# Optimization experiments

Hardware: AMD Instinct MI355X
Metric: run time of the kernel (lower is better)

## Reference

```python
import jax, jax.numpy as jnp
import numpy as np

S = 56
BATCH = 3136 * 0 + 256  # batch size
D = 5 * 2 + 20  # 5*B + C = 30 channels per cell
LAMBDA_COORD = 5.0
LAMBDA_NOOBJ = 0.5


def setup_inputs() -> dict:
    key = jax.random.key(0)
    k1, k2, k3 = jax.random.split(key, 3)
    predictions = jax.random.uniform(k1, (BATCH, S, S, D), dtype=jnp.float32,
                                     minval=0.01, maxval=1.0)
    target = jax.random.uniform(k2, (BATCH, S, S, D), dtype=jnp.float32,
                                 minval=0.01, maxval=1.0)
    # objectness channel must be exactly 1.0 or 0.0 (code tests target[...,4] == 1)
    obj = (jax.random.uniform(k3, (BATCH, S, S)) < 0.3).astype(jnp.float32)
    target = target.at[..., 4].set(obj)
    return {"predictions": predictions, "target": target}


def reference(predictions, target):
    # obj mask: cells where target objectness is exactly 1
    obj = (target[..., 4] == 1.0).astype(predictions.dtype)   # [B,S,S]
    noobj = 1.0 - obj

    # coord loss: (x,y) squared diff + (sqrt(w),sqrt(h)) squared diff
    dxy = jnp.sum((predictions[..., 0:2] - target[..., 0:2]) ** 2, axis=-1)
    dwh = jnp.sum((jnp.sqrt(predictions[..., 2:4]) - jnp.sqrt(target[..., 2:4])) ** 2, axis=-1)
    coord = LAMBDA_COORD * (dxy + dwh)

    # confidence squared error (used for both object and no-object terms)
    conf = (predictions[..., 4] - target[..., 4]) ** 2

    # class loss over [5:] (faithful to original slice)
    cls = jnp.sum((predictions[..., 5:] - target[..., 5:]) ** 2, axis=-1)

    per_cell = obj * (coord + conf + cls) + noobj * (LAMBDA_NOOBJ * conf)
    return jnp.sum(per_cell) / predictions.shape[0]
```

## Files before the change

kernel.cpp:

```cpp
#include <hip/hip_runtime.h>

#define NBATCH 256
#define NCH 30
#define UF 4

__device__ __forceinline__ float fast_sqrt(float x) {
    float r;
    asm("v_sqrt_f32 %0, %1" : "=v"(r) : "v"(x));
    return r;
}

__global__ __launch_bounds__(256, 4) void yolo_loss_uf_kernel(
    const float* __restrict__ pred,
    const float* __restrict__ targ,
    float* __restrict__ out,
    int n4)
{
    const int nthreads = gridDim.x * blockDim.x;
    const int tid = blockIdx.x * blockDim.x + threadIdx.x;

    const int e0    = tid * 4;
    const int c0    = e0 % NCH;
    const int cell0 = e0 / NCH;
    const int hioff = (c0 + 3 >= NCH) ? NCH : 0;
    const int dconf = nthreads * 4;

    float A[4], B[4];
    bool  SQ[4], LO[4];
    #pragma unroll
    for (int k = 0; k < 4; ++k) {
        int c = c0 + k; if (c >= NCH) c -= NCH;
        SQ[k] = (c == 2 || c == 3);
        LO[k] = (c0 + k) < NCH;
        if (c < 4)       { A[k] = 5.0f; B[k] = 0.0f; }
        else if (c == 4) { A[k] = 0.5f; B[k] = 0.5f; }
        else             { A[k] = 1.0f; B[k] = 0.0f; }
    }

    const float4* __restrict__ p4 = reinterpret_cast<const float4*>(pred);
    const float4* __restrict__ t4 = reinterpret_cast<const float4*>(targ);
    const float*  __restrict__ cb = targ + (size_t)cell0 * NCH + 4;

    float acc = 0.0f;
    int i = tid;
    size_t coff = 0;

    const int nmain = n4 / (nthreads * UF);
    for (int su = 0; su < nmain; ++su) {
        float4 pv[UF], tv[UF];
        float  clo[UF], chi[UF];
        #pragma unroll
        for (int u = 0; u < UF; ++u) pv[u] = p4[i + u * nthreads];
        #pragma unroll
        for (int u = 0; u < UF; ++u) tv[u] = t4[i + u * nthreads];
        #pragma unroll
        for (int u = 0; u < UF; ++u) {
            clo[u] = cb[coff + (size_t)u * dconf];
            chi[u] = cb[coff + (size_t)u * dconf + hioff];
        }

        #pragma unroll
        for (int u = 0; u < UF; ++u) {
            float obj_lo = (clo[u] == 1.0f) ? 1.0f : 0.0f;
            float obj_hi = (chi[u] == 1.0f) ? 1.0f : 0.0f;
            float pe[4] = {pv[u].x, pv[u].y, pv[u].z, pv[u].w};
            float te[4] = {tv[u].x, tv[u].y, tv[u].z, tv[u].w};
            #pragma unroll
            for (int k = 0; k < 4; ++k) {
                float p = pe[k], t = te[k];
                float dp = p - t;
                float ds = fast_sqrt(p) - fast_sqrt(t);
                float d   = SQ[k] ? ds : dp;
                float obj = LO[k] ? obj_lo : obj_hi;
                float w   = fmaf(obj, A[k], B[k]);
                acc = fmaf(w * d, d, acc);
            }
        }
        i    += UF * nthreads;
        coff += (size_t)UF * dconf;
    }

    for (; i < n4; i += nthreads, coff += dconf) {
        float4 pv = p4[i];
        float4 tv = t4[i];
        float obj_lo = (cb[coff] == 1.0f) ? 1.0f : 0.0f;
        float obj_hi = (cb[coff + hioff] == 1.0f) ? 1.0f : 0.0f;
        float pe[4] = {pv.x, pv.y, pv.z, pv.w};
        float te[4] = {tv.x, tv.y, tv.z, tv.w};
        #pragma unroll
        for (int k = 0; k < 4; ++k) {
            float p = pe[k], t = te[k];
            float dp = p - t;
            float ds = fast_sqrt(p) - fast_sqrt(t);
            float d   = SQ[k] ? ds : dp;
            float obj = LO[k] ? obj_lo : obj_hi;
            float w   = fmaf(obj, A[k], B[k]);
            acc = fmaf(w * d, d, acc);
        }
    }

    #pragma unroll
    for (int off = 32; off > 0; off >>= 1)
        acc += __shfl_down(acc, off, 64);

    __shared__ float lds[4];
    int lane = threadIdx.x & 63;
    int wid  = threadIdx.x >> 6;
    if (lane == 0) lds[wid] = acc;
    __syncthreads();
    if (threadIdx.x == 0) {
        float s = lds[0] + lds[1] + lds[2] + lds[3];
        atomicAdd(out, s * (1.0f / (float)NBATCH));
    }
}

extern "C" void kernel_launch(void* const* d_in, const int* in_sizes, int n_in,
                              void* d_out, int out_size, void* d_ws, size_t ws_size,
                              hipStream_t stream)
{
    const float* pred = (const float*)d_in[0];
    const float* targ = (const float*)d_in[1];
    float* out = (float*)d_out;

    hipMemsetAsync(out, 0, sizeof(float), stream);

    int n  = in_sizes[0];
    int n4 = n / 4;

    int blocks = 1470;
    yolo_loss_uf_kernel<<<blocks, 256, 0, stream>>>(pred, targ, out, n4);
}
```

Baseline: 43.16 us.

## Fetch objectness flags via wavefront shuffles instead of scalar global reloads

After: 93.91 us. 118% more time.

```diff
diff --git a/kernel.cpp b/kernel.cpp
--- a/kernel.cpp
+++ b/kernel.cpp
@@ -10,7 +10,7 @@
     return r;
 }
 
-__global__ __launch_bounds__(256, 4) void yolo_loss_uf_kernel(
+__global__ __launch_bounds__(256, 4) void yolo_loss_kernel(
     const float* __restrict__ pred,
     const float* __restrict__ targ,
     float* __restrict__ out,
@@ -22,8 +22,16 @@
     const int e0    = tid * 4;
     const int c0    = e0 % NCH;
     const int cell0 = e0 / NCH;
-    const int hioff = (c0 + 3 >= NCH) ? NCH : 0;
-    const int dconf = nthreads * 4;
+    const int cellh = (e0 + 3) / NCH;
+    const int Flo0  = cell0 * NCH + 4;
+    const int Fhi0  = cellh * NCH + 4;
+    const int hlo   = Flo0 >> 2;
+    const int hhi   = Fhi0 >> 2;
+    const int lane_lo = hlo & 63;
+    const int lane_hi = hhi & 63;
+    const bool inw_lo = (hlo >> 6) == (tid >> 6);
+    const bool inw_hi = (hhi >> 6) == (tid >> 6);
+    const int k_sel = (4 - c0 + NCH) % NCH;
 
     float A[4], B[4];
     bool  SQ[4], LO[4];
@@ -39,32 +47,34 @@
 
     const float4* __restrict__ p4 = reinterpret_cast<const float4*>(pred);
     const float4* __restrict__ t4 = reinterpret_cast<const float4*>(targ);
-    const float*  __restrict__ cb = targ + (size_t)cell0 * NCH + 4;
 
     float acc = 0.0f;
     int i = tid;
-    size_t coff = 0;
+    int foff = 0;
 
     const int nmain = n4 / (nthreads * UF);
     for (int su = 0; su < nmain; ++su) {
         float4 pv[UF], tv[UF];
-        float  clo[UF], chi[UF];
         #pragma unroll
         for (int u = 0; u < UF; ++u) pv[u] = p4[i + u * nthreads];
         #pragma unroll
         for (int u = 0; u < UF; ++u) tv[u] = t4[i + u * nthreads];
-        #pragma unroll
-        for (int u = 0; u < UF; ++u) {
-            clo[u] = cb[coff + (size_t)u * dconf];
-            chi[u] = cb[coff + (size_t)u * dconf + hioff];
-        }
 
         #pragma unroll
         for (int u = 0; u < UF; ++u) {
-            float obj_lo = (clo[u] == 1.0f) ? 1.0f : 0.0f;
-            float obj_hi = (chi[u] == 1.0f) ? 1.0f : 0.0f;
             float pe[4] = {pv[u].x, pv[u].y, pv[u].z, pv[u].w};
             float te[4] = {tv[u].x, tv[u].y, tv[u].z, tv[u].w};
+            float sel = te[0];
+            sel = (k_sel == 1) ? te[1] : sel;
+            sel = (k_sel == 2) ? te[2] : sel;
+            sel = (k_sel == 3) ? te[3] : sel;
+            float clo = __shfl(sel, lane_lo, 64);
+            float chi = __shfl(sel, lane_hi, 64);
+            const int off_u = foff + 4 * u * nthreads;
+            if (!inw_lo) clo = targ[Flo0 + off_u];
+            if (!inw_hi) chi = targ[Fhi0 + off_u];
+            float obj_lo = (clo == 1.0f) ? 1.0f : 0.0f;
+            float obj_hi = (chi == 1.0f) ? 1.0f : 0.0f;
             #pragma unroll
             for (int k = 0; k < 4; ++k) {
                 float p = pe[k], t = te[k];
@@ -77,14 +87,17 @@
             }
         }
         i    += UF * nthreads;
-        coff += (size_t)UF * dconf;
+        foff += 4 * UF * nthreads;
     }
 
-    for (; i < n4; i += nthreads, coff += dconf) {
+    for (; i < n4; i += nthreads) {
+        const int off = i * 4 - e0;
         float4 pv = p4[i];
         float4 tv = t4[i];
-        float obj_lo = (cb[coff] == 1.0f) ? 1.0f : 0.0f;
-        float obj_hi = (cb[coff + hioff] == 1.0f) ? 1.0f : 0.0f;
+        float clo = targ[Flo0 + off];
+        float chi = targ[Fhi0 + off];
+        float obj_lo = (clo == 1.0f) ? 1.0f : 0.0f;
+        float obj_hi = (chi == 1.0f) ? 1.0f : 0.0f;
         float pe[4] = {pv.x, pv.y, pv.z, pv.w};
         float te[4] = {tv.x, tv.y, tv.z, tv.w};
         #pragma unroll
@@ -127,6 +140,6 @@
     int n  = in_sizes[0];
     int n4 = n / 4;
 
-    int blocks = 1470;
-    yolo_loss_uf_kernel<<<blocks, 256, 0, stream>>>(pred, targ, out, n4);
+    int blocks = 5880;
+    yolo_loss_kernel<<<blocks, 256, 0, stream>>>(pred, targ, out, n4);
 }
```
